# Kernel tuning notes

Measured on AMD Instinct MI355X. Metric: run time of the kernel, lower is better.

Reference implementation:

```python
import jax, jax.numpy as jnp
import numpy as np

INPUT_DIM = 512
EMBED_DIM = 64
B, S = 4, 4096


def setup_inputs() -> dict:
    key = jax.random.key(0)
    ks = jax.random.split(key, 9)
    scale = 1.0 / np.sqrt(INPUT_DIM)
    return {
        "q": jax.random.normal(ks[0], (B, S, INPUT_DIM), dtype=jnp.float32),
        "k": jax.random.normal(ks[1], (B, S, INPUT_DIM), dtype=jnp.float32),
        "v": jax.random.normal(ks[2], (B, S, INPUT_DIM), dtype=jnp.float32),
        "Wq": jax.random.uniform(ks[3], (INPUT_DIM, EMBED_DIM), jnp.float32, -scale, scale),
        "bq": jax.random.uniform(ks[4], (EMBED_DIM,), jnp.float32, -scale, scale),
        "Wk": jax.random.uniform(ks[5], (INPUT_DIM, EMBED_DIM), jnp.float32, -scale, scale),
        "bk": jax.random.uniform(ks[6], (EMBED_DIM,), jnp.float32, -scale, scale),
        "Wv": jax.random.uniform(ks[7], (INPUT_DIM, EMBED_DIM), jnp.float32, -scale, scale),
        "bv": jax.random.uniform(ks[8], (EMBED_DIM,), jnp.float32, -scale, scale),
    }


def reference(q, k, v, Wq, bq, Wk, bk, Wv, bv):
    # Linear projections (torch Linear: x @ W^T + b; here W stored as [in, out])
    Q = q @ Wq + bq  # [B, S, E]
    K = k @ Wk + bk  # [B, S, E]
    V = v @ Wv + bv  # [B, S, E]
    d_k = K.shape[-1]
    scores = jnp.einsum("bqe,bke->bqk", Q, K) / jnp.sqrt(jnp.float32(d_k))  # [B, S, S]
    attn = jax.nn.softmax(scores, axis=-1)
    return jnp.einsum("bqk,bke->bqe", attn, V)  # [B, S, E]
```

## Files before the change

kernel.cpp:

```cpp
#include <hip/hip_runtime.h>
#include <math.h>

#define S_ 4096
#define C_SCALE 0.18033688011112042f
#define KSPLIT 8

typedef __attribute__((ext_vector_type(4))) float  floatx4;
typedef __attribute__((ext_vector_type(4))) short  short4_t;
typedef __attribute__((ext_vector_type(8))) short  short8_t;
typedef __attribute__((ext_vector_type(2))) unsigned int uintx2;
typedef __attribute__((ext_vector_type(4))) unsigned int uintx4;

__device__ __forceinline__ short f2bf(float f) {
  unsigned u = __builtin_bit_cast(unsigned, f);
  u += 0x7FFFu + ((u >> 16) & 1u);
  return (short)(u >> 16);
}
__device__ __forceinline__ unsigned pack2(float lo, float hi) {
  unsigned a = __builtin_bit_cast(unsigned, lo) + 0x8000u;
  unsigned b = __builtin_bit_cast(unsigned, hi) + 0x8000u;
  return __builtin_amdgcn_perm(b, a, 0x07060302u);
}
__device__ __forceinline__ unsigned packt(float lo, float hi) {
  return __builtin_amdgcn_perm(__builtin_bit_cast(unsigned, hi),
                               __builtin_bit_cast(unsigned, lo), 0x07060302u);
}
__device__ __forceinline__ float bf2f(short s) {
  return __builtin_bit_cast(float, (unsigned)((unsigned short)s) << 16);
}
__device__ __forceinline__ void dma16(const void* g, void* l) {
  __builtin_amdgcn_global_load_lds(
      (const __attribute__((address_space(1))) void*)g,
      (__attribute__((address_space(3))) void*)l, 16, 0, 0);
}

__global__ __launch_bounds__(256) void prep_w(const float* __restrict__ Wq,
                                              const float* __restrict__ Wk,
                                              const float* __restrict__ Wv,
                                              short* __restrict__ Wt) {
  __shared__ float T[64 * 65];
  int m = blockIdx.x >> 3, kt = blockIdx.x & 7, tid = threadIdx.x;
  const float* W = (m == 0) ? Wq : (m == 1) ? Wk : Wv;
  float sc = (m == 0) ? C_SCALE : 1.0f;
#pragma unroll
  for (int i = 0; i < 16; i++) {
    int e = i * 256 + tid;
    int k = e >> 6, n = e & 63;
    T[k * 65 + n] = W[(kt * 64 + k) * 64 + n];
  }
  __syncthreads();
#pragma unroll
  for (int i = 0; i < 16; i++) {
    int e = i * 256 + tid;
    int n = e >> 6, k = e & 63;
    Wt[m * 32768 + n * 512 + kt * 64 + k] = f2bf(T[k * 65 + n] * sc);
  }
}

__global__ __launch_bounds__(256, 3) void proj_kernel(
    const float* __restrict__ qin, const float* __restrict__ kin,
    const float* __restrict__ vin, const float* __restrict__ bq,
    const float* __restrict__ bk, const float* __restrict__ bv,
    const short* __restrict__ Wt, short* __restrict__ Qp,
    short* __restrict__ Kp, short* __restrict__ Vt) {
  __shared__ short A_lds[64 * 64];
  __shared__ short W_lds[64 * 64];

  int tid = threadIdx.x;
  int m = blockIdx.x >> 8;
  int r0 = (blockIdx.x & 255) * 64;
  int wid = tid >> 6, lane = tid & 63, l15 = lane & 15, quad = lane >> 4;

  const float* in = (m == 0) ? qin : (m == 1) ? kin : vin;
  const short* Wm = Wt + m * 32768;

  int sr = tid >> 3, sc = tid & 7;
  int sphys = ((sc ^ (sr & 7)) * 8);

  floatx4 ar[4];
  auto loadA = [&](int kc) {
    const float* p = in + (size_t)(r0 + sr) * 512 + kc * 64 + sc * 8;
    ar[0] = *(const floatx4*)p;
    ar[1] = *(const floatx4*)(p + 4);
    const float* p2 = p + 32 * 512;
    ar[2] = *(const floatx4*)p2;
    ar[3] = *(const floatx4*)(p2 + 4);
  };
  auto dmaW = [&](int kc) {
#pragma unroll
    for (int j = 0; j < 2; j++) {
      int slot = wid * 128 + j * 64 + lane;
      int r = slot >> 3, c = slot & 7;
      int gc = (c ^ (r & 7)) * 8;
      dma16(Wm + r * 512 + kc * 64 + gc, (void*)&W_lds[(wid * 2 + j) * 512]);
    }
  };

  floatx4 acc[4];
#pragma unroll
  for (int nb = 0; nb < 4; nb++) acc[nb] = (floatx4){0.f, 0.f, 0.f, 0.f};

  loadA(0);
#pragma unroll
  for (int kc = 0; kc < 8; kc++) {
    if (kc) __syncthreads();
    dmaW(kc);
    uintx4 w0 = {pack2(ar[0][0], ar[0][1]), pack2(ar[0][2], ar[0][3]),
                 pack2(ar[1][0], ar[1][1]), pack2(ar[1][2], ar[1][3])};
    uintx4 w1 = {pack2(ar[2][0], ar[2][1]), pack2(ar[2][2], ar[2][3]),
                 pack2(ar[3][0], ar[3][1]), pack2(ar[3][2], ar[3][3])};
    *(short8_t*)(A_lds + sr * 64 + sphys) = __builtin_bit_cast(short8_t, w0);
    *(short8_t*)(A_lds + (sr + 32) * 64 + sphys) = __builtin_bit_cast(short8_t, w1);
    if (kc < 7) loadA(kc + 1);
    __syncthreads();
    int arow = wid * 16 + l15;
    int akey = arow & 7, wkey = l15 & 7;
#pragma unroll
    for (int h = 0; h < 2; h++) {
      short8_t af = *(const short8_t*)(A_lds + arow * 64 + ((h * 4 + quad) ^ akey) * 8);
#pragma unroll
      for (int nb = 0; nb < 4; nb++) {
        short8_t wf = *(const short8_t*)(W_lds + (nb * 16 + l15) * 64 +
                                         ((h * 4 + quad) ^ wkey) * 8);
        acc[nb] = __builtin_amdgcn_mfma_f32_16x16x32_bf16(af, wf, acc[nb], 0, 0, 0);
      }
    }
  }

  const float* bias = (m == 0) ? bq : (m == 1) ? bk : bv;
  float bsc = (m == 0) ? C_SCALE : 1.0f;
  if (m < 2) {
    short* out = (m == 0) ? Qp : Kp;
#pragma unroll
    for (int nb = 0; nb < 4; nb++) {
      float bv_ = bias[nb * 16 + l15] * bsc;
#pragma unroll
      for (int r = 0; r < 4; r++)
        out[(size_t)(r0 + wid * 16 + quad * 4 + r) * 64 + nb * 16 + l15] =
            f2bf(acc[nb][r] + bv_);
    }
  } else {
    int bb = r0 >> 12;
    int s0 = (r0 & 4095) + wid * 16 + quad * 4;
#pragma unroll
    for (int nb = 0; nb < 4; nb++) {
      float bv_ = bias[nb * 16 + l15];
      short4_t pk = {f2bf(acc[nb][0] + bv_), f2bf(acc[nb][1] + bv_),
                     f2bf(acc[nb][2] + bv_), f2bf(acc[nb][3] + bv_)};
      *(short4_t*)(Vt + (size_t)bb * 262144 + (nb * 16 + l15) * 4096 + s0) = pk;
    }
  }
}

__global__ __launch_bounds__(256, 2) void attn_kernel(
    const short* __restrict__ Qp, const short* __restrict__ Kp,
    const short* __restrict__ Vt, short* __restrict__ Po,
    float* __restrict__ Lp) {
  __shared__ short K_lds[2][64 * 64];
  __shared__ short V_lds[2][64 * 64];
  __shared__ short P_lds[4][64 * 64];

  int tid = threadIdx.x;
  int ks = blockIdx.x >> 6, b = (blockIdx.x >> 4) & 3, qt = blockIdx.x & 15;
  int wid = tid >> 6, lane = tid & 63, l15 = lane & 15, quad = lane >> 4;
  int key = l15 & 7;

  const short* Qb = Qp + (size_t)b * (S_ * 64);
  const short* Kb = Kp + (size_t)b * (S_ * 64);
  const short* Vb = Vt + (size_t)b * (64 * S_);

  int q0 = qt * 256 + wid * 64;

  short8_t qf[4][2];
#pragma unroll
  for (int qs = 0; qs < 4; qs++)
#pragma unroll
    for (int h = 0; h < 2; h++)
      qf[qs][h] = *(const short8_t*)(Qb + (q0 + qs * 16 + l15) * 64 + h * 32 + quad * 8);

  floatx4 o[4][4];
#pragma unroll
  for (int qs = 0; qs < 4; qs++)
#pragma unroll
    for (int eb = 0; eb < 4; eb++) o[qs][eb] = (floatx4){0.f, 0.f, 0.f, 0.f};
  float l_acc[4] = {0.f, 0.f, 0.f, 0.f};
  short* Pw = &P_lds[wid][0];
  int ks_base = ks * 512;

  auto stage = [&](int t, int buf) {
    int ks0 = ks_base + t * 64;
#pragma unroll
    for (int j = 0; j < 2; j++) {
      int slot = wid * 128 + j * 64 + lane;
      int r = slot >> 3, c = slot & 7;
      int gc = (c ^ (r & 7)) * 8;
      dma16(Kb + (ks0 + r) * 64 + gc, (void*)&K_lds[buf][(wid * 2 + j) * 512]);
      dma16(Vb + (size_t)r * 4096 + ks0 + gc, (void*)&V_lds[buf][(wid * 2 + j) * 512]);
    }
  };

  stage(0, 0);
  for (int t = 0; t < 8; t++) {
    __syncthreads();
    if (t < 7) stage(t + 1, (t + 1) & 1);
    __syncthreads();
    const short* Kt = K_lds[t & 1];
    const short* Vl = V_lds[t & 1];

#pragma unroll
    for (int jh = 0; jh < 2; jh++) {
      short8_t kA[4];
#pragma unroll
      for (int jb = 0; jb < 2; jb++)
#pragma unroll
        for (int eh = 0; eh < 2; eh++)
          kA[jb * 2 + eh] = *(const short8_t*)(
              Kt + (jh * 32 + jb * 16 + l15) * 64 + ((eh * 4 + quad) ^ key) * 8);

#pragma unroll
      for (int qs = 0; qs < 4; qs++) {
        floatx4 z = (floatx4){0.f, 0.f, 0.f, 0.f};
        floatx4 s0 = __builtin_amdgcn_mfma_f32_16x16x32_bf16(kA[0], qf[qs][0], z, 0, 0, 0);
        s0 = __builtin_amdgcn_mfma_f32_16x16x32_bf16(kA[1], qf[qs][1], s0, 0, 0, 0);
        floatx4 s1 = __builtin_amdgcn_mfma_f32_16x16x32_bf16(kA[2], qf[qs][0], z, 0, 0, 0);
        s1 = __builtin_amdgcn_mfma_f32_16x16x32_bf16(kA[3], qf[qs][1], s1, 0, 0, 0);
        float e00 = __builtin_amdgcn_exp2f(s0[0]), e01 = __builtin_amdgcn_exp2f(s0[1]);
        float e02 = __builtin_amdgcn_exp2f(s0[2]), e03 = __builtin_amdgcn_exp2f(s0[3]);
        float e10 = __builtin_amdgcn_exp2f(s1[0]), e11 = __builtin_amdgcn_exp2f(s1[1]);
        float e12 = __builtin_amdgcn_exp2f(s1[2]), e13 = __builtin_amdgcn_exp2f(s1[3]);
        l_acc[qs] += ((e00 + e01) + (e02 + e03)) + ((e10 + e11) + (e12 + e13));
        int row = (qs * 16 + l15) * 64;
        uintx2 w0 = {packt(e00, e01), packt(e02, e03)};
        uintx2 w1 = {packt(e10, e11), packt(e12, e13)};
        *(uintx2*)(Pw + row + ((jh * 4 + 0 + (quad >> 1)) ^ key) * 8 + (quad & 1) * 4) = w0;
        *(uintx2*)(Pw + row + ((jh * 4 + 2 + (quad >> 1)) ^ key) * 8 + (quad & 1) * 4) = w1;
      }

      short8_t pf[4];
#pragma unroll
      for (int qs = 0; qs < 4; qs++)
        pf[qs] = *(const short8_t*)(Pw + (qs * 16 + l15) * 64 +
                                    ((jh * 4 + quad) ^ key) * 8);
#pragma unroll
      for (int eb = 0; eb < 4; eb++) {
        short8_t vf = *(const short8_t*)(Vl + (eb * 16 + l15) * 64 +
                                         ((jh * 4 + quad) ^ key) * 8);
#pragma unroll
        for (int qs = 0; qs < 4; qs++)
          o[qs][eb] = __builtin_amdgcn_mfma_f32_16x16x32_bf16(pf[qs], vf, o[qs][eb], 0, 0, 0);
      }
    }
  }

#pragma unroll
  for (int qs = 0; qs < 4; qs++) {
    float l = l_acc[qs];
    l += __shfl_xor(l, 16, 64);
    l += __shfl_xor(l, 32, 64);
    int grow_base = b * 4096 + q0 + qs * 16;
    short* Pb = Po + ((size_t)ks * 16384 + grow_base) * 64;
#pragma unroll
    for (int eb = 0; eb < 4; eb++)
#pragma unroll
      for (int r = 0; r < 4; r++)
        Pb[(size_t)(quad * 4 + r) * 64 + eb * 16 + l15] = f2bf(o[qs][eb][r]);
    if (quad == 0) Lp[ks * 16384 + grow_base + l15] = l;
  }
}

__global__ __launch_bounds__(256) void combine_kernel(
    const short* __restrict__ Po, const float* __restrict__ Lp,
    float* __restrict__ out) {
  int gid = blockIdx.x * 256 + threadIdx.x;
  int grow = gid >> 3, e0 = (gid & 7) * 8;
  float s[8];
#pragma unroll
  for (int i = 0; i < 8; i++) s[i] = 0.f;
  float l = 0.f;
#pragma unroll
  for (int ks = 0; ks < KSPLIT; ks++) {
    short8_t p = *(const short8_t*)(Po + ((size_t)ks * 16384 + grow) * 64 + e0);
#pragma unroll
    for (int i = 0; i < 8; i++) s[i] += bf2f(p[i]);
    l += Lp[ks * 16384 + grow];
  }
  float inv = 1.0f / l;
  floatx4 o0 = {s[0] * inv, s[1] * inv, s[2] * inv, s[3] * inv};
  floatx4 o1 = {s[4] * inv, s[5] * inv, s[6] * inv, s[7] * inv};
  *(floatx4*)(out + (size_t)grow * 64 + e0) = o0;
  *(floatx4*)(out + (size_t)grow * 64 + e0 + 4) = o1;
}

extern "C" void kernel_launch(void* const* d_in, const int* in_sizes, int n_in,
                              void* d_out, int out_size, void* d_ws, size_t ws_size,
                              hipStream_t stream) {
  const float* q = (const float*)d_in[0];
  const float* k = (const float*)d_in[1];
  const float* v = (const float*)d_in[2];
  const float* Wq = (const float*)d_in[3];
  const float* bq = (const float*)d_in[4];
  const float* Wk = (const float*)d_in[5];
  const float* bk = (const float*)d_in[6];
  const float* Wv = (const float*)d_in[7];
  const float* bv = (const float*)d_in[8];

  char* ws = (char*)d_ws;
  short* Qp = (short*)(ws);
  short* Kp = (short*)(ws + (1u << 21));
  short* Vt = (short*)(ws + (2u << 21));
  short* Wt = (short*)(ws + (3u << 21));
  short* Po = (short*)(ws + (4u << 21));
  float* Lp = (float*)(ws + (13u << 21));

  prep_w<<<24, 256, 0, stream>>>(Wq, Wk, Wv, Wt);
  proj_kernel<<<768, 256, 0, stream>>>(q, k, v, bq, bk, bv, Wt, Qp, Kp, Vt);
  attn_kernel<<<512, 256, 0, stream>>>(Qp, Kp, Vt, Po, Lp);
  combine_kernel<<<512, 256, 0, stream>>>(Po, Lp, (float*)d_out);
}
```

Baseline: 165.3 us.

## Keep softmax probabilities in registers and hold projection weights in VGPRs

The attention kernel now computes transposed scores with a permuted K row order, so the exponentiated probabilities already sit in the MFMA B-operand layout. They feed the PV MFMA directly, which drops the P round-trip through LDS and the LDS buffer. The projection kernel preloads each wave's weight slice into registers instead of DMAing W tiles every k-step, and double-buffers the A tile so one barrier per step suffices. The cost is higher register pressure from the preloaded weights and more complex swizzle indexing.

```diff
diff --git a/kernel.cpp b/kernel.cpp
--- a/kernel.cpp
+++ b/kernel.cpp
@@ -8,7 +8,6 @@
 typedef __attribute__((ext_vector_type(4))) float  floatx4;
 typedef __attribute__((ext_vector_type(4))) short  short4_t;
 typedef __attribute__((ext_vector_type(8))) short  short8_t;
-typedef __attribute__((ext_vector_type(2))) unsigned int uintx2;
 typedef __attribute__((ext_vector_type(4))) unsigned int uintx4;
 
 __device__ __forceinline__ short f2bf(float f) {
@@ -63,8 +62,7 @@
     const float* __restrict__ bk, const float* __restrict__ bv,
     const short* __restrict__ Wt, short* __restrict__ Qp,
     short* __restrict__ Kp, short* __restrict__ Vt) {
-  __shared__ short A_lds[64 * 64];
-  __shared__ short W_lds[64 * 64];
+  __shared__ short A_lds[2][64 * 64];
 
   int tid = threadIdx.x;
   int m = blockIdx.x >> 8;
@@ -74,8 +72,16 @@
   const float* in = (m == 0) ? qin : (m == 1) ? kin : vin;
   const short* Wm = Wt + m * 32768;
 
+  short8_t wf[8][2];
+#pragma unroll
+  for (int kc = 0; kc < 8; kc++)
+#pragma unroll
+    for (int eh = 0; eh < 2; eh++)
+      wf[kc][eh] = *(const short8_t*)(Wm + (wid * 16 + l15) * 512 + kc * 64 +
+                                      eh * 32 + quad * 8);
+
   int sr = tid >> 3, sc = tid & 7;
-  int sphys = ((sc ^ (sr & 7)) * 8);
+  int sphys = (sc ^ (sr & 7)) * 8;
 
   floatx4 ar[4];
   auto loadA = [&](int kc) {
@@ -86,68 +92,55 @@
     ar[2] = *(const floatx4*)p2;
     ar[3] = *(const floatx4*)(p2 + 4);
   };
-  auto dmaW = [&](int kc) {
-#pragma unroll
-    for (int j = 0; j < 2; j++) {
-      int slot = wid * 128 + j * 64 + lane;
-      int r = slot >> 3, c = slot & 7;
-      int gc = (c ^ (r & 7)) * 8;
-      dma16(Wm + r * 512 + kc * 64 + gc, (void*)&W_lds[(wid * 2 + j) * 512]);
-    }
-  };
 
   floatx4 acc[4];
 #pragma unroll
-  for (int nb = 0; nb < 4; nb++) acc[nb] = (floatx4){0.f, 0.f, 0.f, 0.f};
+  for (int rt = 0; rt < 4; rt++) acc[rt] = (floatx4){0.f, 0.f, 0.f, 0.f};
 
   loadA(0);
 #pragma unroll
   for (int kc = 0; kc < 8; kc++) {
-    if (kc) __syncthreads();
-    dmaW(kc);
     uintx4 w0 = {pack2(ar[0][0], ar[0][1]), pack2(ar[0][2], ar[0][3]),
                  pack2(ar[1][0], ar[1][1]), pack2(ar[1][2], ar[1][3])};
     uintx4 w1 = {pack2(ar[2][0], ar[2][1]), pack2(ar[2][2], ar[2][3]),
                  pack2(ar[3][0], ar[3][1]), pack2(ar[3][2], ar[3][3])};
-    *(short8_t*)(A_lds + sr * 64 + sphys) = __builtin_bit_cast(short8_t, w0);
-    *(short8_t*)(A_lds + (sr + 32) * 64 + sphys) = __builtin_bit_cast(short8_t, w1);
+    short* Ab = &A_lds[kc & 1][0];
+    *(short8_t*)(Ab + sr * 64 + sphys) = __builtin_bit_cast(short8_t, w0);
+    *(short8_t*)(Ab + (sr + 32) * 64 + sphys) = __builtin_bit_cast(short8_t, w1);
+    __syncthreads();
     if (kc < 7) loadA(kc + 1);
-    __syncthreads();
-    int arow = wid * 16 + l15;
-    int akey = arow & 7, wkey = l15 & 7;
-#pragma unroll
-    for (int h = 0; h < 2; h++) {
-      short8_t af = *(const short8_t*)(A_lds + arow * 64 + ((h * 4 + quad) ^ akey) * 8);
-#pragma unroll
-      for (int nb = 0; nb < 4; nb++) {
-        short8_t wf = *(const short8_t*)(W_lds + (nb * 16 + l15) * 64 +
-                                         ((h * 4 + quad) ^ wkey) * 8);
-        acc[nb] = __builtin_amdgcn_mfma_f32_16x16x32_bf16(af, wf, acc[nb], 0, 0, 0);
+    int akey = l15 & 7;
+#pragma unroll
+    for (int rt = 0; rt < 4; rt++) {
+      int arow = rt * 16 + l15;
+#pragma unroll
+      for (int eh = 0; eh < 2; eh++) {
+        short8_t af = *(const short8_t*)(Ab + arow * 64 + ((eh * 4 + quad) ^ akey) * 8);
+        acc[rt] = __builtin_amdgcn_mfma_f32_16x16x32_bf16(af, wf[kc][eh], acc[rt], 0, 0, 0);
       }
     }
   }
 
   const float* bias = (m == 0) ? bq : (m == 1) ? bk : bv;
   float bsc = (m == 0) ? C_SCALE : 1.0f;
+  float bv_ = bias[wid * 16 + l15] * bsc;
   if (m < 2) {
     short* out = (m == 0) ? Qp : Kp;
 #pragma unroll
-    for (int nb = 0; nb < 4; nb++) {
-      float bv_ = bias[nb * 16 + l15] * bsc;
+    for (int rt = 0; rt < 4; rt++)
 #pragma unroll
       for (int r = 0; r < 4; r++)
-        out[(size_t)(r0 + wid * 16 + quad * 4 + r) * 64 + nb * 16 + l15] =
-            f2bf(acc[nb][r] + bv_);
-    }
+        out[(size_t)(r0 + rt * 16 + quad * 4 + r) * 64 + wid * 16 + l15] =
+            f2bf(acc[rt][r] + bv_);
   } else {
     int bb = r0 >> 12;
-    int s0 = (r0 & 4095) + wid * 16 + quad * 4;
-#pragma unroll
-    for (int nb = 0; nb < 4; nb++) {
-      float bv_ = bias[nb * 16 + l15];
-      short4_t pk = {f2bf(acc[nb][0] + bv_), f2bf(acc[nb][1] + bv_),
-                     f2bf(acc[nb][2] + bv_), f2bf(acc[nb][3] + bv_)};
-      *(short4_t*)(Vt + (size_t)bb * 262144 + (nb * 16 + l15) * 4096 + s0) = pk;
+    int s0 = (r0 & 4095);
+#pragma unroll
+    for (int rt = 0; rt < 4; rt++) {
+      short4_t pk = {f2bf(acc[rt][0] + bv_), f2bf(acc[rt][1] + bv_),
+                     f2bf(acc[rt][2] + bv_), f2bf(acc[rt][3] + bv_)};
+      *(short4_t*)(Vt + (size_t)bb * 262144 + (wid * 16 + l15) * 4096 + s0 +
+                   rt * 16 + quad * 4) = pk;
     }
   }
 }
@@ -158,12 +151,10 @@
     float* __restrict__ Lp) {
   __shared__ short K_lds[2][64 * 64];
   __shared__ short V_lds[2][64 * 64];
-  __shared__ short P_lds[4][64 * 64];
 
   int tid = threadIdx.x;
   int ks = blockIdx.x >> 6, b = (blockIdx.x >> 4) & 3, qt = blockIdx.x & 15;
   int wid = tid >> 6, lane = tid & 63, l15 = lane & 15, quad = lane >> 4;
-  int key = l15 & 7;
 
   const short* Qb = Qp + (size_t)b * (S_ * 64);
   const short* Kb = Kp + (size_t)b * (S_ * 64);
@@ -184,7 +175,6 @@
 #pragma unroll
     for (int eb = 0; eb < 4; eb++) o[qs][eb] = (floatx4){0.f, 0.f, 0.f, 0.f};
   float l_acc[4] = {0.f, 0.f, 0.f, 0.f};
-  short* Pw = &P_lds[wid][0];
   int ks_base = ks * 512;
 
   auto stage = [&](int t, int buf) {
@@ -193,9 +183,10 @@
     for (int j = 0; j < 2; j++) {
       int slot = wid * 128 + j * 64 + lane;
       int r = slot >> 3, c = slot & 7;
-      int gc = (c ^ (r & 7)) * 8;
-      dma16(Kb + (ks0 + r) * 64 + gc, (void*)&K_lds[buf][(wid * 2 + j) * 512]);
-      dma16(Vb + (size_t)r * 4096 + ks0 + gc, (void*)&V_lds[buf][(wid * 2 + j) * 512]);
+      int kk = (r & 3) | (((r >> 3) & 1) << 2);
+      dma16(Kb + (ks0 + r) * 64 + (c ^ kk) * 8, (void*)&K_lds[buf][(wid * 2 + j) * 512]);
+      dma16(Vb + (size_t)r * 4096 + ks0 + (c ^ (r & 7)) * 8,
+            (void*)&V_lds[buf][(wid * 2 + j) * 512]);
     }
   };
 
@@ -207,47 +198,39 @@
     const short* Kt = K_lds[t & 1];
     const short* Vl = V_lds[t & 1];
 
-#pragma unroll
-    for (int jh = 0; jh < 2; jh++) {
-      short8_t kA[4];
-#pragma unroll
-      for (int jb = 0; jb < 2; jb++)
-#pragma unroll
-        for (int eh = 0; eh < 2; eh++)
-          kA[jb * 2 + eh] = *(const short8_t*)(
-              Kt + (jh * 32 + jb * 16 + l15) * 64 + ((eh * 4 + quad) ^ key) * 8);
-
+    int pr = 8 * (l15 >> 2) + (l15 & 3);
+    int kkey = (l15 & 3) | (((l15 >> 2) & 1) << 2);
+
+#pragma unroll
+    for (int jg = 0; jg < 2; jg++) {
+      const short* Kg = Kt + (jg * 32 + pr) * 64;
+      short8_t kA0 = *(const short8_t*)(Kg + ((0 + quad) ^ kkey) * 8);
+      short8_t kA1 = *(const short8_t*)(Kg + ((4 + quad) ^ kkey) * 8);
+      short8_t kA2 = *(const short8_t*)(Kg + 256 + ((0 + quad) ^ kkey) * 8);
+      short8_t kA3 = *(const short8_t*)(Kg + 256 + ((4 + quad) ^ kkey) * 8);
+      short8_t vf[4];
+#pragma unroll
+      for (int eb = 0; eb < 4; eb++)
+        vf[eb] = *(const short8_t*)(Vl + (eb * 16 + l15) * 64 +
+                                    ((jg * 4 + quad) ^ (l15 & 7)) * 8);
 #pragma unroll
       for (int qs = 0; qs < 4; qs++) {
         floatx4 z = (floatx4){0.f, 0.f, 0.f, 0.f};
-        floatx4 s0 = __builtin_amdgcn_mfma_f32_16x16x32_bf16(kA[0], qf[qs][0], z, 0, 0, 0);
-        s0 = __builtin_amdgcn_mfma_f32_16x16x32_bf16(kA[1], qf[qs][1], s0, 0, 0, 0);
-        floatx4 s1 = __builtin_amdgcn_mfma_f32_16x16x32_bf16(kA[2], qf[qs][0], z, 0, 0, 0);
-        s1 = __builtin_amdgcn_mfma_f32_16x16x32_bf16(kA[3], qf[qs][1], s1, 0, 0, 0);
+        floatx4 s0 = __builtin_amdgcn_mfma_f32_16x16x32_bf16(kA0, qf[qs][0], z, 0, 0, 0);
+        s0 = __builtin_amdgcn_mfma_f32_16x16x32_bf16(kA1, qf[qs][1], s0, 0, 0, 0);
+        floatx4 s1 = __builtin_amdgcn_mfma_f32_16x16x32_bf16(kA2, qf[qs][0], z, 0, 0, 0);
+        s1 = __builtin_amdgcn_mfma_f32_16x16x32_bf16(kA3, qf[qs][1], s1, 0, 0, 0);
         float e00 = __builtin_amdgcn_exp2f(s0[0]), e01 = __builtin_amdgcn_exp2f(s0[1]);
         float e02 = __builtin_amdgcn_exp2f(s0[2]), e03 = __builtin_amdgcn_exp2f(s0[3]);
         float e10 = __builtin_amdgcn_exp2f(s1[0]), e11 = __builtin_amdgcn_exp2f(s1[1]);
         float e12 = __builtin_amdgcn_exp2f(s1[2]), e13 = __builtin_amdgcn_exp2f(s1[3]);
         l_acc[qs] += ((e00 + e01) + (e02 + e03)) + ((e10 + e11) + (e12 + e13));
-        int row = (qs * 16 + l15) * 64;
-        uintx2 w0 = {packt(e00, e01), packt(e02, e03)};
-        uintx2 w1 = {packt(e10, e11), packt(e12, e13)};
-        *(uintx2*)(Pw + row + ((jh * 4 + 0 + (quad >> 1)) ^ key) * 8 + (quad & 1) * 4) = w0;
-        *(uintx2*)(Pw + row + ((jh * 4 + 2 + (quad >> 1)) ^ key) * 8 + (quad & 1) * 4) = w1;
-      }
-
-      short8_t pf[4];
-#pragma unroll
-      for (int qs = 0; qs < 4; qs++)
-        pf[qs] = *(const short8_t*)(Pw + (qs * 16 + l15) * 64 +
-                                    ((jh * 4 + quad) ^ key) * 8);
-#pragma unroll
-      for (int eb = 0; eb < 4; eb++) {
-        short8_t vf = *(const short8_t*)(Vl + (eb * 16 + l15) * 64 +
-                                         ((jh * 4 + quad) ^ key) * 8);
-#pragma unroll
-        for (int qs = 0; qs < 4; qs++)
-          o[qs][eb] = __builtin_amdgcn_mfma_f32_16x16x32_bf16(pf[qs], vf, o[qs][eb], 0, 0, 0);
+        uintx4 bp = {packt(e00, e01), packt(e02, e03),
+                     packt(e10, e11), packt(e12, e13)};
+        short8_t pB = __builtin_bit_cast(short8_t, bp);
+#pragma unroll
+        for (int eb = 0; eb < 4; eb++)
+          o[qs][eb] = __builtin_amdgcn_mfma_f32_16x16x32_bf16(vf[eb], pB, o[qs][eb], 0, 0, 0);
       }
     }
   }
@@ -257,14 +240,15 @@
     float l = l_acc[qs];
     l += __shfl_xor(l, 16, 64);
     l += __shfl_xor(l, 32, 64);
-    int grow_base = b * 4096 + q0 + qs * 16;
-    short* Pb = Po + ((size_t)ks * 16384 + grow_base) * 64;
-#pragma unroll
-    for (int eb = 0; eb < 4; eb++)
-#pragma unroll
-      for (int r = 0; r < 4; r++)
-        Pb[(size_t)(quad * 4 + r) * 64 + eb * 16 + l15] = f2bf(o[qs][eb][r]);
-    if (quad == 0) Lp[ks * 16384 + grow_base + l15] = l;
+    int grow = b * 4096 + q0 + qs * 16 + l15;
+    short* Pb = Po + ((size_t)ks * 16384 + grow) * 64;
+#pragma unroll
+    for (int eb = 0; eb < 4; eb++) {
+      short4_t pk = {f2bf(o[qs][eb][0]), f2bf(o[qs][eb][1]),
+                     f2bf(o[qs][eb][2]), f2bf(o[qs][eb][3])};
+      *(short4_t*)(Pb + eb * 16 + quad * 4) = pk;
+    }
+    if (quad == 0) Lp[ks * 16384 + grow] = l;
   }
 }
 
```

New measurement: 168.3 us. Within noise of the previous version (+1.8%).
